# Performance work log

Hardware: AMD Instinct MI355X
Metric: run time of the kernel (lower is better)

## Reference

```python
import jax, jax.numpy as jnp
import numpy as np

BATCH_SIZE = 1024  # init kwarg: Pair(batch_size)
D = 260            # per-item feature dim; last 4 entries are (x1, y1, x2, y2)


def setup_inputs() -> dict:
    key = jax.random.key(0)
    k_feat, k_xy, k_wh = jax.random.split(key, 3)
    feats = jax.random.normal(k_feat, (1, BATCH_SIZE, D - 4), dtype=jnp.float32)
    # Valid boxes: x2 > x1, y2 > y1 so areas are strictly positive (avoids div-by-zero,
    # matching the intended use on real detector boxes).
    xy1 = jax.random.uniform(k_xy, (1, BATCH_SIZE, 2), minval=0.0, maxval=0.5)
    wh = jax.random.uniform(k_wh, (1, BATCH_SIZE, 2), minval=0.05, maxval=0.5)
    bbox = jnp.concatenate([xy1, xy1 + wh], axis=-1)  # (x1, y1, x2, y2)
    inputs = jnp.concatenate([feats, bbox], axis=-1).astype(jnp.float32)
    return {"inputs": inputs}


def reference(inputs) -> jnp.ndarray:
    n = inputs.shape[1] // 2          # loops run over range(batch_size // 2)
    d = inputs.shape[2]
    x = inputs[0, :n]                 # [n, D] — only first half of rows is used
    x1, y1, x2, y2 = x[:, -4], x[:, -3], x[:, -2], x[:, -1]
    area = (x2 - x1) * (y2 - y1)      # [n]
    # Pairwise intersection, all (i, j) at once.
    w = jnp.maximum(0.0, jnp.minimum(x2[:, None], x2[None, :]) - jnp.maximum(x1[:, None], x1[None, :]))
    h = jnp.maximum(0.0, jnp.minimum(y2[:, None], y2[None, :]) - jnp.maximum(y1[:, None], y1[None, :]))
    inter = w * h                     # [n, n]
    r1 = inter / area[:, None]        # intersection / area_i
    r2 = inter / area[None, :]        # intersection / area_j
    xi = jnp.broadcast_to(x[:, None, :], (n, n, d))  # features of i
    xj = jnp.broadcast_to(x[None, :, :], (n, n, d))  # features of j
    out = jnp.concatenate([xi, xj, r1[..., None], r2[..., None]], axis=-1)  # [n, n, 2D+2]
    # Original appends in i-outer, j-inner order then concats on axis 1.
    return out.reshape(1, n * n, 2 * d + 2)
```

## Files before the change

### kernel.cpp

```cpp
#include <hip/hip_runtime.h>


#define N 512
#define D 260
#define JT 16
#define ROW 522
#define REG_F4 (JT * ROW / 4)

__global__ __launch_bounds__(256) void pair_kernel(const float* __restrict__ in,
                                                   float* __restrict__ out) {
    const int b    = blockIdx.x;
    const int i    = b >> 5;
    const int j0   = (b & 31) * JT;
    const int tid  = threadIdx.x;
    const int lane = tid & 63;
    const int w    = tid >> 6;

    __shared__ __align__(16) float s_img[JT * ROW];

    const float* rowi = in + i * D;
    const float2 xi_a = ((const float2*)rowi)[lane];
    const float2 xi_b = ((const float2*)rowi)[64 + lane];
    const float4 bb   = *(const float4*)(rowi + 256);

    for (int lj = w; lj < JT; lj += 4) {
        const float* xjrow = in + (size_t)(j0 + lj) * D;
        const float2 ga = ((const float2*)xjrow)[lane];
        const float2 gb = ((const float2*)xjrow)[64 + lane];
        float2* row2 = (float2*)(s_img + lj * ROW);

        row2[lane]       = xi_a;
        row2[64 + lane]  = xi_b;
        row2[130 + lane] = ga;
        row2[194 + lane] = gb;
        if (lane < 2) {
            row2[128 + lane] = lane ? make_float2(bb.z, bb.w)
                                    : make_float2(bb.x, bb.y);
            row2[258 + lane] = ((const float2*)xjrow)[128 + lane];
        }
        if (lane == 2) {
            const float4 bj = *(const float4*)(xjrow + 256);
            const float ww = fmaxf(0.0f, fminf(bb.z, bj.z) - fmaxf(bb.x, bj.x));
            const float hh = fmaxf(0.0f, fminf(bb.w, bj.w) - fmaxf(bb.y, bj.y));
            const float inter = ww * hh;
            row2[260] = make_float2(inter / ((bb.z - bb.x) * (bb.w - bb.y)),
                                    inter / ((bj.z - bj.x) * (bj.w - bj.y)));
        }
    }
    __syncthreads();

    const float4* s4 = (const float4*)s_img;
    float4* o4 = (float4*)(out + (size_t)(i * N + j0) * ROW);

    int t = tid;
    #pragma unroll
    for (int k = 0; k < 8; ++k, t += 256) {
        o4[t] = s4[t];
    }
    if (t < REG_F4) o4[t] = s4[t];
}

extern "C" void kernel_launch(void* const* d_in, const int* in_sizes, int n_in,
                              void* d_out, int out_size, void* d_ws, size_t ws_size,
                              hipStream_t stream) {
    const float* in = (const float*)d_in[0];
    float* out = (float*)d_out;
    pair_kernel<<<N * (N / JT), 256, 0, stream>>>(in, out);
}
```

Before: 530.0 us.

## Replace LDS-staged tiles with persistent grid-stride float2 gather and software pipelining

Drops the shared-memory staging of 16-row output tiles. A fixed grid of 2048 blocks instead walks the flat output as float2 elements, computing each source address by magic-number division (row = m/261). Loads and stores are double-buffered in groups of four to overlap reads of the small L2-resident input with streaming writes. The aim is to remove the LDS round trip and the barrier and to keep writes fully coalesced. The cost is per-element index arithmetic, float2-wide stores instead of float4, and scattered gathers from the input.

```diff
diff --git a/kernel.cpp b/kernel.cpp
--- a/kernel.cpp
+++ b/kernel.cpp
@@ -3,61 +3,77 @@
 
 #define N 512
 #define D 260
-#define JT 16
-#define ROW 522
-#define REG_F4 (JT * ROW / 4)
+#define RPF2 261
+#define TOTF2 (N * N * RPF2)
+#define NBLK 2048
+#define NTHR 256
+#define TT (NBLK * NTHR)
 
-__global__ __launch_bounds__(256) void pair_kernel(const float* __restrict__ in,
-                                                   float* __restrict__ out) {
-    const int b    = blockIdx.x;
-    const int i    = b >> 5;
-    const int j0   = (b & 31) * JT;
-    const int tid  = threadIdx.x;
-    const int lane = tid & 63;
-    const int w    = tid >> 6;
+__device__ __forceinline__ float2 pair_src(const float* __restrict__ in, unsigned m) {
+    const unsigned row = (unsigned)(((unsigned long long)m * 65823254ull) >> 34);
+    const unsigned s   = m - row * RPF2;
+    const unsigned i   = row >> 9;
+    const unsigned j   = row & (N - 1);
 
-    __shared__ __align__(16) float s_img[JT * ROW];
+    const bool     fi  = (s < 130u);
+    const unsigned sj  = s - 130u;
+    const unsigned ri  = fi ? i : j;
+    const unsigned off = fi ? s : (sj < 130u ? sj : 0u);
+    float2 v = *(const float2*)(in + ri * D + 2u * off);
 
-    const float* rowi = in + i * D;
-    const float2 xi_a = ((const float2*)rowi)[lane];
-    const float2 xi_b = ((const float2*)rowi)[64 + lane];
-    const float4 bb   = *(const float4*)(rowi + 256);
+    if (s == 260u) {
+        const float* bi = in + i * D + 256;
+        const float* bj = in + j * D + 256;
+        const float2 bi0 = *(const float2*)bi, bi1 = *(const float2*)(bi + 2);
+        const float2 bj0 = *(const float2*)bj, bj1 = *(const float2*)(bj + 2);
+        const float ww = fmaxf(0.f, fminf(bi1.x, bj1.x) - fmaxf(bi0.x, bj0.x));
+        const float hh = fmaxf(0.f, fminf(bi1.y, bj1.y) - fmaxf(bi0.y, bj0.y));
+        const float inter = ww * hh;
+        v = make_float2(inter / ((bi1.x - bi0.x) * (bi1.y - bi0.y)),
+                        inter / ((bj1.x - bj0.x) * (bj1.y - bj0.y)));
+    }
+    return v;
+}
 
-    for (int lj = w; lj < JT; lj += 4) {
-        const float* xjrow = in + (size_t)(j0 + lj) * D;
-        const float2 ga = ((const float2*)xjrow)[lane];
-        const float2 gb = ((const float2*)xjrow)[64 + lane];
-        float2* row2 = (float2*)(s_img + lj * ROW);
+__global__ __launch_bounds__(NTHR) void pair_kernel(const float* __restrict__ in,
+                                                    float* __restrict__ out) {
+    const unsigned T = blockIdx.x * NTHR + threadIdx.x;
+    float2* __restrict__ o2 = (float2*)out;
 
-        row2[lane]       = xi_a;
-        row2[64 + lane]  = xi_b;
-        row2[130 + lane] = ga;
-        row2[194 + lane] = gb;
-        if (lane < 2) {
-            row2[128 + lane] = lane ? make_float2(bb.z, bb.w)
-                                    : make_float2(bb.x, bb.y);
-            row2[258 + lane] = ((const float2*)xjrow)[128 + lane];
-        }
-        if (lane == 2) {
-            const float4 bj = *(const float4*)(xjrow + 256);
-            const float ww = fmaxf(0.0f, fminf(bb.z, bj.z) - fmaxf(bb.x, bj.x));
-            const float hh = fmaxf(0.0f, fminf(bb.w, bj.w) - fmaxf(bb.y, bj.y));
-            const float inter = ww * hh;
-            row2[260] = make_float2(inter / ((bb.z - bb.x) * (bb.w - bb.y)),
-                                    inter / ((bj.z - bj.x) * (bj.w - bj.y)));
-        }
+    float2 a0, a1, a2, a3, b0, b1, b2, b3;
+
+#define LOADG(r0, r1, r2, r3, q)                          \
+    r0 = pair_src(in, (unsigned)(4 * (q) + 0) * TT + T);  \
+    r1 = pair_src(in, (unsigned)(4 * (q) + 1) * TT + T);  \
+    r2 = pair_src(in, (unsigned)(4 * (q) + 2) * TT + T);  \
+    r3 = pair_src(in, (unsigned)(4 * (q) + 3) * TT + T);
+#define STORG(r0, r1, r2, r3, q)                          \
+    o2[(unsigned)(4 * (q) + 0) * TT + T] = r0;            \
+    o2[(unsigned)(4 * (q) + 1) * TT + T] = r1;            \
+    o2[(unsigned)(4 * (q) + 2) * TT + T] = r2;            \
+    o2[(unsigned)(4 * (q) + 3) * TT + T] = r3;
+
+    LOADG(a0, a1, a2, a3, 0)
+    LOADG(b0, b1, b2, b3, 1)
+    STORG(a0, a1, a2, a3, 0)
+
+    #pragma unroll 1
+    for (int t = 0; t < 15; ++t) {
+        const int q = 2 * t + 2;
+        LOADG(a0, a1, a2, a3, q)
+        STORG(b0, b1, b2, b3, q - 1)
+        LOADG(b0, b1, b2, b3, q + 1)
+        STORG(a0, a1, a2, a3, q)
     }
-    __syncthreads();
+    STORG(b0, b1, b2, b3, 31)
 
-    const float4* s4 = (const float4*)s_img;
-    float4* o4 = (float4*)(out + (size_t)(i * N + j0) * ROW);
-
-    int t = tid;
-    #pragma unroll
-    for (int k = 0; k < 8; ++k, t += 256) {
-        o4[t] = s4[t];
+    #pragma unroll 1
+    for (unsigned k = 128; k <= 130; ++k) {
+        const unsigned m = k * TT + T;
+        if (m < TOTF2) o2[m] = pair_src(in, m);
     }
-    if (t < REG_F4) o4[t] = s4[t];
+#undef LOADG
+#undef STORG
 }
 
 extern "C" void kernel_launch(void* const* d_in, const int* in_sizes, int n_in,
@@ -65,5 +81,5 @@
                               hipStream_t stream) {
     const float* in = (const float*)d_in[0];
     float* out = (float*)d_out;
-    pair_kernel<<<N * (N / JT), 256, 0, stream>>>(in, out);
+    pair_kernel<<<NBLK, NTHR, 0, stream>>>(in, out);
 }
```

New measurement: 547.8 us. +3.4%, slower.
